# Performance work log

Measured on AMD Instinct MI355X. Metric: run time of the kernel, lower is better.

The kernel has to match this reference:

```python
import jax, jax.numpy as jnp
import numpy as np
from jax import lax

B, T, F, K = 128, 1024, 128, 32


def setup_inputs() -> dict:
    key = jax.random.key(0)
    k1, k2, k3 = jax.random.split(key, 3)
    inp = jax.random.normal(k1, (B, T, F), dtype=jnp.float32)
    mask = jnp.ones((B, T), dtype=bool)
    W_emit = jax.random.normal(k2, (F, K), dtype=jnp.float32) * 0.02
    transition = jax.random.normal(k3, (K, K), dtype=jnp.float32) * 0.1
    return {"input": inp, "mask": mask, "W_emit": W_emit, "transition": transition}


def reference(input, mask, W_emit, transition):
    # emissions: [B, T, K]
    emission = jnp.einsum('btf,fk->btk', input, W_emit)
    alpha0 = emission[:, 0]                      # [B, K]
    em_seq = jnp.swapaxes(emission[:, 1:], 0, 1)  # [T-1, B, K]
    mk_seq = jnp.swapaxes(mask[:, 1:], 0, 1)      # [T-1, B]

    def step(alpha, xs):
        em_t, m_t = xs
        # alpha_t[b,j] = logsumexp_i(alpha[b,i] + transition[i,j]) + em_t[b,j]
        new = jax.scipy.special.logsumexp(alpha[:, :, None] + transition[None], axis=1) + em_t
        alpha = jnp.where(m_t[:, None], new, alpha)
        return alpha, None

    alpha, _ = lax.scan(step, alpha0, (em_seq, mk_seq))
    log_z = jax.scipy.special.logsumexp(alpha, axis=-1)  # [B]
    return jnp.sum(log_z)
```

## Files before the change

### kernel.cpp

```cpp
#include <hip/hip_runtime.h>
#include <hip/hip_bf16.h>

#define Bb 128
#define Tt 1024
#define Ff 128
#define Kk 32
#define KS 36
#define KE 36
#define LOG32 3.4657359027997265f

typedef __attribute__((ext_vector_type(8))) short bf16x8;
typedef __attribute__((ext_vector_type(4))) float f32x4;

__device__ __forceinline__ float bf2f(unsigned u) {
    return __uint_as_float(u << 16);
}
__device__ __forceinline__ unsigned short f2bf(float f) {
    unsigned u = __float_as_uint(f);
    u = (u + 0x7fffu + ((u >> 16) & 1u)) >> 16;
    return (unsigned short)u;
}
__device__ __forceinline__ unsigned bfpk2(float a, float b) {
    __hip_bfloat162 h = __float22bfloat162_rn(make_float2(a, b));
    unsigned u;
    __builtin_memcpy(&u, &h, sizeof(u));
    return u;
}

__global__ __launch_bounds__(64, 4) void chunk_kernel(
    const float* __restrict__ inp, const int* __restrict__ mask,
    const float* __restrict__ W, const float* __restrict__ trans,
    unsigned short* __restrict__ SQ, float* __restrict__ out)
{
    __shared__ __align__(16) float gl[32 * KE];
    __shared__ __align__(16) unsigned short Sl[32 * KS];
    const int lane = threadIdx.x & 63;
    const int q = lane >> 4, n = lane & 15;
    const int b = blockIdx.x >> 5, c = blockIdx.x & 31;
    const int t0 = c * 32;

    if (blockIdx.x == 0 && lane == 0) out[0] = 0.f;

    const int* mbp = mask + (long)b * Tt;
    int mybit = (lane < 32) ? (mbp[t0 + lane] != 0) : 0;
    unsigned mbits = (unsigned)__ballot(mybit);
    if (c == 0) mbits &= ~1u;

    bf16x8 A0, A1;
    #pragma unroll
    for (int j = 0; j < 8; ++j) {
        A0[j] = (short)f2bf(__expf(trans[(q * 8 + j) * Kk + n]));
        A1[j] = (short)f2bf(__expf(trans[(q * 8 + j) * Kk + 16 + n]));
    }

    const f32x4 zz = {0.f, 0.f, 0.f, 0.f};
    f32x4 E00 = zz, E01 = zz, E10 = zz, E11 = zz;
    const float* xrow = inp + ((long)b * Tt + t0) * Ff;
    #pragma unroll
    for (int kt = 0; kt < 4; ++kt) {
        const int f0 = kt * 32 + q * 8;
        float4 al0 = *(const float4*)&xrow[ n        * Ff + f0];
        float4 al1 = *(const float4*)&xrow[ n        * Ff + f0 + 4];
        float4 ah0 = *(const float4*)&xrow[(n + 16)  * Ff + f0];
        float4 ah1 = *(const float4*)&xrow[(n + 16)  * Ff + f0 + 4];
        uint4 ua = make_uint4(bfpk2(al0.x, al0.y), bfpk2(al0.z, al0.w),
                              bfpk2(al1.x, al1.y), bfpk2(al1.z, al1.w));
        uint4 ub = make_uint4(bfpk2(ah0.x, ah0.y), bfpk2(ah0.z, ah0.w),
                              bfpk2(ah1.x, ah1.y), bfpk2(ah1.z, ah1.w));
        bf16x8 Alo = __builtin_bit_cast(bf16x8, ua);
        bf16x8 Ahi = __builtin_bit_cast(bf16x8, ub);
        float wl[8], wh[8];
        #pragma unroll
        for (int jj = 0; jj < 8; ++jj) {
            wl[jj] = W[(f0 + jj) * Kk + n];
            wh[jj] = W[(f0 + jj) * Kk + 16 + n];
        }
        uint4 uc = make_uint4(bfpk2(wl[0], wl[1]), bfpk2(wl[2], wl[3]),
                              bfpk2(wl[4], wl[5]), bfpk2(wl[6], wl[7]));
        uint4 ud = make_uint4(bfpk2(wh[0], wh[1]), bfpk2(wh[2], wh[3]),
                              bfpk2(wh[4], wh[5]), bfpk2(wh[6], wh[7]));
        bf16x8 Blo = __builtin_bit_cast(bf16x8, uc);
        bf16x8 Bhi = __builtin_bit_cast(bf16x8, ud);
        E00 = __builtin_amdgcn_mfma_f32_16x16x32_bf16(Alo, Blo, E00, 0, 0, 0);
        E01 = __builtin_amdgcn_mfma_f32_16x16x32_bf16(Alo, Bhi, E01, 0, 0, 0);
        E10 = __builtin_amdgcn_mfma_f32_16x16x32_bf16(Ahi, Blo, E10, 0, 0, 0);
        E11 = __builtin_amdgcn_mfma_f32_16x16x32_bf16(Ahi, Bhi, E11, 0, 0, 0);
    }
    #pragma unroll
    for (int r = 0; r < 4; ++r) {
        gl[( q * 4 + r)      * KE + n]      = __expf(E00[r] - LOG32);
        gl[( q * 4 + r)      * KE + 16 + n] = __expf(E01[r] - LOG32);
        gl[(16 + q * 4 + r)  * KE + n]      = __expf(E10[r] - LOG32);
        gl[(16 + q * 4 + r)  * KE + 16 + n] = __expf(E11[r] - LOG32);
    }

    for (int i = lane; i < (32 * KS) / 2; i += 64)
        ((unsigned*)Sl)[i] = 0u;
    if (lane < 32) Sl[lane * KS + lane] = 0x3f80;

    #pragma unroll
    for (int s = 0; s < 32; ++s) {
        if (!((mbits >> s) & 1u)) continue;
        uint2 xa = *(const uint2*)&Sl[ n       * KS + q * 8];
        uint2 xb = *(const uint2*)&Sl[ n       * KS + q * 8 + 4];
        uint2 ya = *(const uint2*)&Sl[(n + 16) * KS + q * 8];
        uint2 yb = *(const uint2*)&Sl[(n + 16) * KS + q * 8 + 4];
        uint4 u0 = make_uint4(xa.x, xa.y, xb.x, xb.y);
        uint4 u1 = make_uint4(ya.x, ya.y, yb.x, yb.y);
        bf16x8 B0 = __builtin_bit_cast(bf16x8, u0);
        bf16x8 B1 = __builtin_bit_cast(bf16x8, u1);
        f32x4 D00 = __builtin_amdgcn_mfma_f32_16x16x32_bf16(A0, B0, zz, 0, 0, 0);
        f32x4 D01 = __builtin_amdgcn_mfma_f32_16x16x32_bf16(A0, B1, zz, 0, 0, 0);
        f32x4 D10 = __builtin_amdgcn_mfma_f32_16x16x32_bf16(A1, B0, zz, 0, 0, 0);
        f32x4 D11 = __builtin_amdgcn_mfma_f32_16x16x32_bf16(A1, B1, zz, 0, 0, 0);
        float4 g0 = *(const float4*)&gl[s * KE + q * 4];
        float4 g1 = *(const float4*)&gl[s * KE + 16 + q * 4];
        *(uint2*)&Sl[ n       * KS      + q * 4] =
            make_uint2(bfpk2(D00[0] * g0.x, D00[1] * g0.y), bfpk2(D00[2] * g0.z, D00[3] * g0.w));
        *(uint2*)&Sl[(n + 16) * KS      + q * 4] =
            make_uint2(bfpk2(D01[0] * g0.x, D01[1] * g0.y), bfpk2(D01[2] * g0.z, D01[3] * g0.w));
        *(uint2*)&Sl[ n       * KS + 16 + q * 4] =
            make_uint2(bfpk2(D10[0] * g1.x, D10[1] * g1.y), bfpk2(D10[2] * g1.z, D10[3] * g1.w));
        *(uint2*)&Sl[(n + 16) * KS + 16 + q * 4] =
            make_uint2(bfpk2(D11[0] * g1.x, D11[1] * g1.y), bfpk2(D11[2] * g1.z, D11[3] * g1.w));
    }

    unsigned short* sq = SQ + (long)(b * 32 + c) * 1024;
    #pragma unroll
    for (int it = 0; it < 2; ++it) {
        int f = it * 512 + lane * 8;
        int kk = f >> 5, n0 = f & 31;
        unsigned v[4];
        #pragma unroll
        for (int e = 0; e < 4; ++e) {
            unsigned lo = Sl[(n0 + 2 * e    ) * KS + kk];
            unsigned hi = Sl[(n0 + 2 * e + 1) * KS + kk];
            v[e] = lo | (hi << 16);
        }
        *(uint4*)(sq + f) = make_uint4(v[0], v[1], v[2], v[3]);
    }
}

__global__ __launch_bounds__(64) void apply_kernel(
    const float* __restrict__ inp, const int* __restrict__ mask,
    const float* __restrict__ W, const unsigned short* __restrict__ SQ,
    float* __restrict__ out)
{
    const int b = blockIdx.x, lane = threadIdx.x & 63, k = lane & 31;
    const int* mbp = mask + (long)b * Tt;

    const unsigned short* sqb = SQ + (long)b * 32 * 1024;
    uint4 cur[4], nxt[4];
    #pragma unroll
    for (int e = 0; e < 4; ++e) cur[e] = *(const uint4*)(sqb + k * 32 + 8 * e);
    #pragma unroll
    for (int e = 0; e < 4; ++e) nxt[e] = *(const uint4*)(sqb + 1024 + k * 32 + 8 * e);

    int cnt = 0;
    #pragma unroll
    for (int it = 0; it < 16; ++it) cnt += (mbp[it * 64 + lane] != 0) ? 1 : 0;
    #pragma unroll
    for (int off = 32; off; off >>= 1) cnt += __shfl_xor(cnt, off);
    cnt -= (mbp[0] != 0) ? 1 : 0;

    const float* x0 = inp + (long)b * Tt * Ff;
    float a0 = 0.f;
    #pragma unroll 4
    for (int f = 0; f < Ff; ++f)
        a0 = fmaf(x0[f], W[f * Kk + k], a0);

    float c0 = __int_as_float(__builtin_amdgcn_readlane(__float_as_int(a0), 0));
    float p = __expf(a0 - c0);
    float csum = c0 + (float)cnt * LOG32;

    #pragma unroll 2
    for (int c = 0; c < 32; ++c) {
        uint4 pf[4];
        if (c + 2 < 32) {
            const unsigned short* s2 = sqb + (c + 2) * 1024 + k * 32;
            #pragma unroll
            for (int e = 0; e < 4; ++e) pf[e] = *(const uint4*)(s2 + 8 * e);
        }
        const int pi = __float_as_int(p);
        float q0 = 0.f, q1 = 0.f, q2 = 0.f, q3 = 0.f;
        #define RL(j) __int_as_float(__builtin_amdgcn_readlane(pi, (j)))
        #define ACC2(word, j, acc) \
            acc = fmaf(bf2f((word) & 0xffffu), RL(j), acc); \
            acc = fmaf(bf2f((word) >> 16),     RL((j) + 1), acc);
        ACC2(cur[0].x,  0, q0) ACC2(cur[0].y,  2, q0) ACC2(cur[0].z,  4, q0) ACC2(cur[0].w,  6, q0)
        ACC2(cur[1].x,  8, q1) ACC2(cur[1].y, 10, q1) ACC2(cur[1].z, 12, q1) ACC2(cur[1].w, 14, q1)
        ACC2(cur[2].x, 16, q2) ACC2(cur[2].y, 18, q2) ACC2(cur[2].z, 20, q2) ACC2(cur[2].w, 22, q2)
        ACC2(cur[3].x, 24, q3) ACC2(cur[3].y, 26, q3) ACC2(cur[3].z, 28, q3) ACC2(cur[3].w, 30, q3)
        #undef ACC2
        #undef RL
        float qq = (q0 + q1) + (q2 + q3);
        if (c == 15) {
            float s0 = __int_as_float(__builtin_amdgcn_readlane(__float_as_int(qq), 0));
            csum += __logf(s0);
            qq *= (1.0f / s0);
        }
        p = qq;
        #pragma unroll
        for (int e = 0; e < 4; ++e) { cur[e] = nxt[e]; nxt[e] = pf[e]; }
    }

    float sum = p;
    #pragma unroll
    for (int off = 16; off > 0; off >>= 1)
        sum += __shfl_xor(sum, off);
    if (lane == 0)
        atomicAdd(out, csum + __logf(sum));
}

extern "C" void kernel_launch(void* const* d_in, const int* in_sizes, int n_in,
                              void* d_out, int out_size, void* d_ws, size_t ws_size,
                              hipStream_t stream)
{
    const float* inp   = (const float*)d_in[0];
    const int*   mask  = (const int*)d_in[1];
    const float* W     = (const float*)d_in[2];
    const float* trans = (const float*)d_in[3];
    float* out = (float*)d_out;
    unsigned short* SQ = (unsigned short*)d_ws;

    chunk_kernel<<<dim3(Bb * 32), dim3(64), 0, stream>>>(inp, mask, W, trans, SQ, out);
    apply_kernel<<<dim3(Bb), dim3(64), 0, stream>>>(inp, mask, W, SQ, out);
}
```

Measured before the change: 128.6 us.

## Split each 32-step chunk across two waves and combine with one matmul

Each chunk block now runs two waves, and each wave builds the transition-product matrix for 16 timesteps instead of one wave doing all 32 in sequence. The two partial products are joined with a single extra MFMA after a barrier and written straight to the workspace. This halves the serial dependency chain inside the chunk kernel, at the cost of an extra bf16 rounding step, a block barrier, and twice the shared scratch. The output store is now scalar 16-bit writes instead of vectorised uint4 writes.

```diff
diff --git a/kernel.cpp b/kernel.cpp
--- a/kernel.cpp
+++ b/kernel.cpp
@@ -27,24 +27,25 @@
     return u;
 }
 
-__global__ __launch_bounds__(64, 4) void chunk_kernel(
+__global__ __launch_bounds__(128, 4) void chunk_kernel(
     const float* __restrict__ inp, const int* __restrict__ mask,
     const float* __restrict__ W, const float* __restrict__ trans,
     unsigned short* __restrict__ SQ, float* __restrict__ out)
 {
     __shared__ __align__(16) float gl[32 * KE];
-    __shared__ __align__(16) unsigned short Sl[32 * KS];
-    const int lane = threadIdx.x & 63;
+    __shared__ __align__(16) unsigned short Sl[2][32 * KS];
+    const int tid = threadIdx.x;
+    const int w = tid >> 6, lane = tid & 63;
     const int q = lane >> 4, n = lane & 15;
     const int b = blockIdx.x >> 5, c = blockIdx.x & 31;
-    const int t0 = c * 32;
-
-    if (blockIdx.x == 0 && lane == 0) out[0] = 0.f;
+    const int tw = c * 32 + w * 16;
+
+    if (blockIdx.x == 0 && tid == 0) out[0] = 0.f;
 
     const int* mbp = mask + (long)b * Tt;
-    int mybit = (lane < 32) ? (mbp[t0 + lane] != 0) : 0;
-    unsigned mbits = (unsigned)__ballot(mybit);
-    if (c == 0) mbits &= ~1u;
+    int mybit = (lane < 16) ? (mbp[tw + lane] != 0) : 0;
+    unsigned mbits = (unsigned)__ballot(mybit) & 0xffffu;
+    if (c == 0 && w == 0) mbits &= ~1u;
 
     bf16x8 A0, A1;
     #pragma unroll
@@ -54,21 +55,16 @@
     }
 
     const f32x4 zz = {0.f, 0.f, 0.f, 0.f};
-    f32x4 E00 = zz, E01 = zz, E10 = zz, E11 = zz;
-    const float* xrow = inp + ((long)b * Tt + t0) * Ff;
+    f32x4 E0 = zz, E1 = zz;
+    const float* xrow = inp + ((long)b * Tt + tw) * Ff;
     #pragma unroll
     for (int kt = 0; kt < 4; ++kt) {
         const int f0 = kt * 32 + q * 8;
-        float4 al0 = *(const float4*)&xrow[ n        * Ff + f0];
-        float4 al1 = *(const float4*)&xrow[ n        * Ff + f0 + 4];
-        float4 ah0 = *(const float4*)&xrow[(n + 16)  * Ff + f0];
-        float4 ah1 = *(const float4*)&xrow[(n + 16)  * Ff + f0 + 4];
-        uint4 ua = make_uint4(bfpk2(al0.x, al0.y), bfpk2(al0.z, al0.w),
-                              bfpk2(al1.x, al1.y), bfpk2(al1.z, al1.w));
-        uint4 ub = make_uint4(bfpk2(ah0.x, ah0.y), bfpk2(ah0.z, ah0.w),
-                              bfpk2(ah1.x, ah1.y), bfpk2(ah1.z, ah1.w));
-        bf16x8 Alo = __builtin_bit_cast(bf16x8, ua);
-        bf16x8 Ahi = __builtin_bit_cast(bf16x8, ub);
+        float4 a0v = *(const float4*)&xrow[n * Ff + f0];
+        float4 a1v = *(const float4*)&xrow[n * Ff + f0 + 4];
+        uint4 ua = make_uint4(bfpk2(a0v.x, a0v.y), bfpk2(a0v.z, a0v.w),
+                              bfpk2(a1v.x, a1v.y), bfpk2(a1v.z, a1v.w));
+        bf16x8 Aw = __builtin_bit_cast(bf16x8, ua);
         float wl[8], wh[8];
         #pragma unroll
         for (int jj = 0; jj < 8; ++jj) {
@@ -81,30 +77,27 @@
                               bfpk2(wh[4], wh[5]), bfpk2(wh[6], wh[7]));
         bf16x8 Blo = __builtin_bit_cast(bf16x8, uc);
         bf16x8 Bhi = __builtin_bit_cast(bf16x8, ud);
-        E00 = __builtin_amdgcn_mfma_f32_16x16x32_bf16(Alo, Blo, E00, 0, 0, 0);
-        E01 = __builtin_amdgcn_mfma_f32_16x16x32_bf16(Alo, Bhi, E01, 0, 0, 0);
-        E10 = __builtin_amdgcn_mfma_f32_16x16x32_bf16(Ahi, Blo, E10, 0, 0, 0);
-        E11 = __builtin_amdgcn_mfma_f32_16x16x32_bf16(Ahi, Bhi, E11, 0, 0, 0);
+        E0 = __builtin_amdgcn_mfma_f32_16x16x32_bf16(Aw, Blo, E0, 0, 0, 0);
+        E1 = __builtin_amdgcn_mfma_f32_16x16x32_bf16(Aw, Bhi, E1, 0, 0, 0);
     }
     #pragma unroll
     for (int r = 0; r < 4; ++r) {
-        gl[( q * 4 + r)      * KE + n]      = __expf(E00[r] - LOG32);
-        gl[( q * 4 + r)      * KE + 16 + n] = __expf(E01[r] - LOG32);
-        gl[(16 + q * 4 + r)  * KE + n]      = __expf(E10[r] - LOG32);
-        gl[(16 + q * 4 + r)  * KE + 16 + n] = __expf(E11[r] - LOG32);
-    }
-
+        gl[(w * 16 + q * 4 + r) * KE + n]      = __expf(E0[r] - LOG32);
+        gl[(w * 16 + q * 4 + r) * KE + 16 + n] = __expf(E1[r] - LOG32);
+    }
+
+    unsigned short* Sw = Sl[w];
     for (int i = lane; i < (32 * KS) / 2; i += 64)
-        ((unsigned*)Sl)[i] = 0u;
-    if (lane < 32) Sl[lane * KS + lane] = 0x3f80;
-
-    #pragma unroll
-    for (int s = 0; s < 32; ++s) {
-        if (!((mbits >> s) & 1u)) continue;
-        uint2 xa = *(const uint2*)&Sl[ n       * KS + q * 8];
-        uint2 xb = *(const uint2*)&Sl[ n       * KS + q * 8 + 4];
-        uint2 ya = *(const uint2*)&Sl[(n + 16) * KS + q * 8];
-        uint2 yb = *(const uint2*)&Sl[(n + 16) * KS + q * 8 + 4];
+        ((unsigned*)Sw)[i] = 0u;
+    if (lane < 32) Sw[lane * KS + lane] = 0x3f80;
+
+    #pragma unroll
+    for (int ls = 0; ls < 16; ++ls) {
+        if (!((mbits >> ls) & 1u)) continue;
+        uint2 xa = *(const uint2*)&Sw[ n       * KS + q * 8];
+        uint2 xb = *(const uint2*)&Sw[ n       * KS + q * 8 + 4];
+        uint2 ya = *(const uint2*)&Sw[(n + 16) * KS + q * 8];
+        uint2 yb = *(const uint2*)&Sw[(n + 16) * KS + q * 8 + 4];
         uint4 u0 = make_uint4(xa.x, xa.y, xb.x, xb.y);
         uint4 u1 = make_uint4(ya.x, ya.y, yb.x, yb.y);
         bf16x8 B0 = __builtin_bit_cast(bf16x8, u0);
@@ -113,31 +106,42 @@
         f32x4 D01 = __builtin_amdgcn_mfma_f32_16x16x32_bf16(A0, B1, zz, 0, 0, 0);
         f32x4 D10 = __builtin_amdgcn_mfma_f32_16x16x32_bf16(A1, B0, zz, 0, 0, 0);
         f32x4 D11 = __builtin_amdgcn_mfma_f32_16x16x32_bf16(A1, B1, zz, 0, 0, 0);
-        float4 g0 = *(const float4*)&gl[s * KE + q * 4];
-        float4 g1 = *(const float4*)&gl[s * KE + 16 + q * 4];
-        *(uint2*)&Sl[ n       * KS      + q * 4] =
+        float4 g0 = *(const float4*)&gl[(w * 16 + ls) * KE + q * 4];
+        float4 g1 = *(const float4*)&gl[(w * 16 + ls) * KE + 16 + q * 4];
+        *(uint2*)&Sw[ n       * KS      + q * 4] =
             make_uint2(bfpk2(D00[0] * g0.x, D00[1] * g0.y), bfpk2(D00[2] * g0.z, D00[3] * g0.w));
-        *(uint2*)&Sl[(n + 16) * KS      + q * 4] =
+        *(uint2*)&Sw[(n + 16) * KS      + q * 4] =
             make_uint2(bfpk2(D01[0] * g0.x, D01[1] * g0.y), bfpk2(D01[2] * g0.z, D01[3] * g0.w));
-        *(uint2*)&Sl[ n       * KS + 16 + q * 4] =
+        *(uint2*)&Sw[ n       * KS + 16 + q * 4] =
             make_uint2(bfpk2(D10[0] * g1.x, D10[1] * g1.y), bfpk2(D10[2] * g1.z, D10[3] * g1.w));
-        *(uint2*)&Sl[(n + 16) * KS + 16 + q * 4] =
+        *(uint2*)&Sw[(n + 16) * KS + 16 + q * 4] =
             make_uint2(bfpk2(D11[0] * g1.x, D11[1] * g1.y), bfpk2(D11[2] * g1.z, D11[3] * g1.w));
     }
 
+    __syncthreads();
+
+    const unsigned short* SlA = Sl[0];
+    const unsigned short* SlB = Sl[1];
+    bf16x8 Af;
+    #pragma unroll
+    for (int j = 0; j < 8; ++j)
+        Af[j] = (short)SlB[(q * 8 + j) * KS + w * 16 + n];
+    uint2 xa = *(const uint2*)&SlA[ n       * KS + q * 8];
+    uint2 xb = *(const uint2*)&SlA[ n       * KS + q * 8 + 4];
+    uint2 ya = *(const uint2*)&SlA[(n + 16) * KS + q * 8];
+    uint2 yb = *(const uint2*)&SlA[(n + 16) * KS + q * 8 + 4];
+    uint4 u0 = make_uint4(xa.x, xa.y, xb.x, xb.y);
+    uint4 u1 = make_uint4(ya.x, ya.y, yb.x, yb.y);
+    bf16x8 B0 = __builtin_bit_cast(bf16x8, u0);
+    bf16x8 B1 = __builtin_bit_cast(bf16x8, u1);
+    f32x4 D0 = __builtin_amdgcn_mfma_f32_16x16x32_bf16(Af, B0, zz, 0, 0, 0);
+    f32x4 D1 = __builtin_amdgcn_mfma_f32_16x16x32_bf16(Af, B1, zz, 0, 0, 0);
+
     unsigned short* sq = SQ + (long)(b * 32 + c) * 1024;
     #pragma unroll
-    for (int it = 0; it < 2; ++it) {
-        int f = it * 512 + lane * 8;
-        int kk = f >> 5, n0 = f & 31;
-        unsigned v[4];
-        #pragma unroll
-        for (int e = 0; e < 4; ++e) {
-            unsigned lo = Sl[(n0 + 2 * e    ) * KS + kk];
-            unsigned hi = Sl[(n0 + 2 * e + 1) * KS + kk];
-            v[e] = lo | (hi << 16);
-        }
-        *(uint4*)(sq + f) = make_uint4(v[0], v[1], v[2], v[3]);
+    for (int r = 0; r < 4; ++r) {
+        sq[(w * 16 + q * 4 + r) * 32 + n]      = f2bf(D0[r]);
+        sq[(w * 16 + q * 4 + r) * 32 + 16 + n] = f2bf(D1[r]);
     }
 }
 
@@ -223,6 +227,6 @@
     float* out = (float*)d_out;
     unsigned short* SQ = (unsigned short*)d_ws;
 
-    chunk_kernel<<<dim3(Bb * 32), dim3(64), 0, stream>>>(inp, mask, W, trans, SQ, out);
+    chunk_kernel<<<dim3(Bb * 32), dim3(128), 0, stream>>>(inp, mask, W, trans, SQ, out);
     apply_kernel<<<dim3(Bb), dim3(64), 0, stream>>>(inp, mask, W, SQ, out);
 }
```

Measured after the change: 127.5 us. Within noise of the previous version (-0.8%).
